# Optimization experiments

Measured on AMD Instinct MI355X. Metric: run time of the kernel, lower is better.

## Reference

```python
import jax, jax.numpy as jnp
import numpy as np

B, P, C, O = 16, 19248, 81, 32
POS_THRESH, NEG_THRESH, NEGPOS_RATIO = 0.5, 0.4, 3
BBOX_ALPHA, CONF_ALPHA = 1.5, 1.0
VAR0, VAR1 = 0.1, 0.2  # SSD encoding variances


def setup_inputs() -> dict:
    key = jax.random.key(0)
    ks = jax.random.split(key, 7)
    loc_data = jax.random.normal(ks[0], (B, P, 4), dtype=jnp.float32)
    conf_data = jax.random.normal(ks[1], (B, P, C), dtype=jnp.float32)
    # priors in center form (cx, cy, w, h), all positive
    cxcy = jax.random.uniform(ks[2], (P, 2), minval=0.05, maxval=0.95)
    wh = jax.random.uniform(ks[3], (P, 2), minval=0.05, maxval=0.30)
    priors = jnp.concatenate([cxcy, wh], axis=-1).astype(jnp.float32)
    # gt boxes in point form (x1, y1, x2, y2), valid and inside [0,1]
    gcxcy = jax.random.uniform(ks[4], (B, O, 2), minval=0.1, maxval=0.9)
    gwh = jax.random.uniform(ks[5], (B, O, 2), minval=0.05, maxval=0.4)
    gt_boxes = jnp.clip(jnp.concatenate([gcxcy - gwh / 2, gcxcy + gwh / 2], axis=-1), 0.0, 1.0).astype(jnp.float32)
    gt_labels = jax.random.randint(ks[6], (B, O), 0, C - 1, dtype=jnp.int32)  # 0..79, bg is class 0 after +1
    return {"loc_data": loc_data, "conf_data": conf_data, "priors": priors,
            "gt_boxes": gt_boxes, "gt_labels": gt_labels}


def _point_form(boxes):
    # center form (cx,cy,w,h) -> point form (x1,y1,x2,y2)
    return jnp.concatenate([boxes[:, :2] - boxes[:, 2:] / 2,
                            boxes[:, :2] + boxes[:, 2:] / 2], axis=-1)


def _jaccard(a, b):
    # a: [O,4] point form, b: [P,4] point form -> IoU [O,P]
    lt = jnp.maximum(a[:, None, :2], b[None, :, :2])
    rb = jnp.minimum(a[:, None, 2:], b[None, :, 2:])
    inter = jnp.prod(jnp.clip(rb - lt, 0.0, None), axis=-1)
    area_a = jnp.prod(a[:, 2:] - a[:, :2], axis=-1)[:, None]
    area_b = jnp.prod(b[:, 2:] - b[:, :2], axis=-1)[None, :]
    return inter / (area_a + area_b - inter)


def _encode(matched, priors):
    # matched: [P,4] point form gt; priors: [P,4] center form
    g_cxcy = ((matched[:, :2] + matched[:, 2:]) / 2 - priors[:, :2]) / (VAR0 * priors[:, 2:])
    g_wh = jnp.log((matched[:, 2:] - matched[:, :2]) / priors[:, 2:]) / VAR1
    return jnp.concatenate([g_cxcy, g_wh], axis=-1)


def _match_one(truths, labels, priors):
    # truths: [O,4] point form, labels: [O] int, priors: [P,4] center form
    overlaps = _jaccard(truths, _point_form(priors))          # [O,P]
    best_truth_overlap = overlaps.max(axis=0)                  # [P]
    best_truth_idx = overlaps.argmax(axis=0)                   # [P]
    best_prior_idx = overlaps.argmax(axis=1)                   # [O]
    # ensure every gt is matched to its best prior
    best_truth_overlap = best_truth_overlap.at[best_prior_idx].set(2.0)
    best_truth_idx = best_truth_idx.at[best_prior_idx].set(jnp.arange(truths.shape[0]))
    matched = truths[best_truth_idx]                           # [P,4]
    conf = labels[best_truth_idx] + 1                          # [P]
    conf = jnp.where(best_truth_overlap < POS_THRESH, -1, conf)  # neutral
    conf = jnp.where(best_truth_overlap < NEG_THRESH, 0, conf)   # background
    loc = _encode(matched, priors)                             # [P,4]
    return loc, conf


def _multibox_loss(loc_data, conf_data, priors, gt_boxes, gt_labels):
    loc_t, conf_t = jax.vmap(_match_one, in_axes=(0, 0, None))(gt_boxes, gt_labels, priors)
    pos = conf_t > 0                                           # [B,P]
    # --- localization: smooth L1 on positives ---
    d = jnp.abs(loc_data - loc_t)
    sl1 = jnp.where(d < 1.0, 0.5 * d * d, d - 0.5)
    loss_B = jnp.sum(sl1 * pos[..., None].astype(sl1.dtype)) * BBOX_ALPHA
    # --- OHEM confidence loss ---
    logZ = jax.nn.logsumexp(conf_data, axis=-1)                # [B,P]
    loss_c = logZ - conf_data[..., 0]                          # log_sum_exp - background logit
    loss_c = jnp.where(pos | (conf_t < 0), 0.0, loss_c)
    order = jnp.argsort(-loss_c, axis=1)                       # descending
    idx_rank = jnp.argsort(order, axis=1)                      # rank of each prior
    num_pos = jnp.sum(pos, axis=1, keepdims=True)              # [B,1]
    num_neg = jnp.clip(NEGPOS_RATIO * num_pos, None, P - 1)
    neg = (idx_rank < num_neg) & (~pos) & (conf_t >= 0)
    ce = logZ - jnp.take_along_axis(conf_data, jnp.maximum(conf_t, 0)[..., None], axis=-1)[..., 0]
    loss_C = jnp.sum(ce * (pos | neg).astype(ce.dtype)) * CONF_ALPHA
    total_num_pos = jnp.sum(pos).astype(loc_data.dtype)
    return jnp.stack([loss_B, loss_C]) / total_num_pos


def reference(loc_data, conf_data, priors, gt_boxes, gt_labels):
    return _multibox_loss(loc_data, conf_data, priors, gt_boxes, gt_labels)
```

## Files before the change

### kernel.cpp

```cpp
#include <hip/hip_runtime.h>
#include <math.h>

#define B_ 16
#define P_ 19248
#define C_ 81
#define O_ 32
#define POS_TH 0.5f
#define NEG_TH 0.4f
#define RPB 128
#define TPB 512
#define PQ  4812
#define BP_BLK (B_ * O_ * 4)
#define BT_BPB 76
#define OT 1024
#define NJ 19

__device__ __forceinline__ float sl1(float x) {
    float d = fabsf(x);
    return (d < 1.0f) ? 0.5f * d * d : d - 0.5f;
}

__device__ __forceinline__ float iou_gt_prior(float4 t, float4 pr) {
    float px1 = pr.x - pr.z * 0.5f;
    float py1 = pr.y - pr.w * 0.5f;
    float px2 = pr.x + pr.z * 0.5f;
    float py2 = pr.y + pr.w * 0.5f;
    float ltx = fmaxf(t.x, px1), lty = fmaxf(t.y, py1);
    float rbx = fminf(t.z, px2), rby = fminf(t.w, py2);
    float iw = fmaxf(rbx - ltx, 0.0f), ih = fmaxf(rby - lty, 0.0f);
    float inter = iw * ih;
    float area_t = (t.z - t.x) * (t.w - t.y);
    float area_p = (px2 - px1) * (py2 - py1);
    return inter / (area_t + area_p - inter);
}

template <int PER>
__device__ __forceinline__ void pick_top(const int* __restrict__ h, int kk, int tid,
                                         int* s_bin, int* s_kk, int* wsum) {
    const int lane = tid & 63, wid = tid >> 6;
    const int base = tid * PER;
    int v[PER]; int s = 0;
    #pragma unroll
    for (int j = 0; j < PER; ++j) { v[j] = h[base + j]; s += v[j]; }
    int x = s;
    #pragma unroll
    for (int d = 1; d < 64; d <<= 1) {
        int y = __shfl_down(x, d);
        if (lane + d < 64) x += y;
    }
    if (lane == 0) wsum[wid] = x;
    __syncthreads();
    int above = 0;
    #pragma unroll
    for (int w = 0; w < 16; ++w) if (w > wid) above += wsum[w];
    int T = (x - s) + above;
    if (T < kk && kk <= T + s) {
        int kl = kk - T, cum = 0;
        #pragma unroll
        for (int j = PER - 1; j >= 0; --j) {
            if (cum + v[j] >= kl) { *s_bin = base + j; *s_kk = kl - cum; break; }
            cum += v[j];
        }
    }
    __syncthreads();
}

template <int PER>
__device__ __forceinline__ void pick_bot(const int* __restrict__ h, int kk, int tid,
                                         int* s_bin, int* s_kk, int* wsum) {
    const int lane = tid & 63, wid = tid >> 6;
    const int base = tid * PER;
    int v[PER]; int s = 0;
    #pragma unroll
    for (int j = 0; j < PER; ++j) { v[j] = h[base + j]; s += v[j]; }
    int x = s;
    #pragma unroll
    for (int d = 1; d < 64; d <<= 1) {
        int y = __shfl_up(x, d);
        if (lane >= d) x += y;
    }
    if (lane == 63) wsum[wid] = x;
    __syncthreads();
    int below = 0;
    #pragma unroll
    for (int w = 0; w < 16; ++w) if (w < wid) below += wsum[w];
    int T = (x - s) + below;
    if (T < kk && kk <= T + s) {
        int kl = kk - T, cum = 0;
        #pragma unroll
        for (int j = 0; j < PER; ++j) {
            if (cum + v[j] >= kl) { *s_bin = base + j; *s_kk = kl - cum; break; }
            cum += v[j];
        }
    }
    __syncthreads();
}

__global__ void k_match(const float* __restrict__ priors,
                        const float* __restrict__ gt_boxes,
                        const int* __restrict__ gt_labels,
                        unsigned long long* __restrict__ best_key,
                        float* __restrict__ bt_ov,
                        int* __restrict__ bt_ix,
                        int* __restrict__ bt_lab) {
    const int bid = blockIdx.x;
    if (bid < BP_BLK) {
        int pair = bid >> 2, qtr = bid & 3;
        int b = pair >> 5, o = pair & 31;
        float4 t = ((const float4*)gt_boxes)[b * O_ + o];
        float bestv = -1.0f; int besti = 0;
        int pstart = qtr * PQ;
        for (int p = pstart + threadIdx.x; p < pstart + PQ; p += 256) {
            float4 pr = ((const float4*)priors)[p];
            float v = iou_gt_prior(t, pr);
            if (v > bestv) { bestv = v; besti = p; }
        }
        __shared__ float sv[256];
        __shared__ int   si[256];
        sv[threadIdx.x] = bestv; si[threadIdx.x] = besti;
        __syncthreads();
        for (int s = 128; s > 0; s >>= 1) {
            if (threadIdx.x < s) {
                float ov = sv[threadIdx.x + s]; int oi = si[threadIdx.x + s];
                if (ov > sv[threadIdx.x] ||
                    (ov == sv[threadIdx.x] && oi < si[threadIdx.x])) {
                    sv[threadIdx.x] = ov; si[threadIdx.x] = oi;
                }
            }
            __syncthreads();
        }
        if (threadIdx.x == 0) {
            unsigned long long key =
                ((unsigned long long)__float_as_uint(sv[0]) << 32) |
                (unsigned long long)(0xFFFFFFFFu - (unsigned int)si[0]);
            atomicMax(&best_key[pair], key);
        }
    } else {
        int idx = bid - BP_BLK;
        int b = idx / BT_BPB;
        int p = (idx % BT_BPB) * 256 + threadIdx.x;
        __shared__ float4 gt[O_];
        __shared__ int    gl[O_];
        if (threadIdx.x < O_) {
            gt[threadIdx.x] = ((const float4*)gt_boxes)[b * O_ + threadIdx.x];
            gl[threadIdx.x] = gt_labels[b * O_ + threadIdx.x];
        }
        __syncthreads();
        if (p >= P_) return;
        float4 pr = ((const float4*)priors)[p];
        float bestv = -1.0f; int besti = 0;
        for (int o = 0; o < O_; ++o) {
            float v = iou_gt_prior(gt[o], pr);
            if (v > bestv) { bestv = v; besti = o; }
        }
        size_t bp = (size_t)b * P_ + p;
        bt_ov[bp] = bestv;
        bt_ix[bp] = besti;
        bt_lab[bp] = gl[besti];
    }
}

__global__ __launch_bounds__(TPB, 6) void
k_main(const float* __restrict__ loc_data,
       const float* __restrict__ conf_data,
       const float* __restrict__ priors,
       const float* __restrict__ gt_boxes,
       const int* __restrict__ gt_labels,
       const unsigned long long* __restrict__ best_key,
       const float* __restrict__ bt_ov,
       const int* __restrict__ bt_ix,
       const int* __restrict__ bt_lab,
       float* __restrict__ lossc,
       float* __restrict__ ce_neg,
       int* __restrict__ num_pos,
       float* __restrict__ accum) {
    __shared__ float srow[RPB * C_];
    __shared__ int s_fp[2][O_];
    __shared__ int s_fl[2][O_];
    __shared__ float s_lB, s_ceP;
    __shared__ int s_np0, s_np1;
    const int row0 = blockIdx.x * RPB;
    const int b0 = row0 / P_;
    const int tid = threadIdx.x;
    const int w = tid >> 6;
    if (tid == 0) { s_lB = 0.0f; s_ceP = 0.0f; s_np0 = 0; s_np1 = 0; }

    {
        const float4* src = (const float4*)(conf_data + (size_t)row0 * C_);
        float4* dst4 = (float4*)srow;
        #pragma unroll
        for (int k = 0; k < 5; ++k) {
            __builtin_amdgcn_global_load_lds(
                (const __attribute__((address_space(1))) void*)(src + k * 512 + tid),
                (__attribute__((address_space(3))) void*)(dst4 + k * 512 + (w << 6)),
                16, 0, 0);
        }
        if (tid < 32) {
            __builtin_amdgcn_global_load_lds(
                (const __attribute__((address_space(1))) void*)(src + 2560 + tid),
                (__attribute__((address_space(3))) void*)(dst4 + 2560),
                16, 0, 0);
        }
    }
    if (tid < 2 * O_) {
        int half = tid >> 5, o = tid & 31;
        int bb = b0 + half;
        int fp = -1, fl = 0;
        if (bb < B_) {
            unsigned long long key = best_key[bb * O_ + o];
            fp = (int)(0xFFFFFFFFu - (unsigned int)(key & 0xFFFFFFFFu));
            fl = gt_labels[bb * O_ + o];
        }
        s_fp[half][o] = fp;
        s_fl[half][o] = fl;
    }
    __syncthreads();

    const int r = tid >> 2;
    const int q = tid & 3;
    const int bp = row0 + r;
    const int b = bp / P_;
    const int p = bp - b * P_;
    const float* row = srow + r * C_;
    const int j0 = 20 * q;

    float ma = row[j0], mb = row[j0 + 1], mc = row[j0 + 2], md = row[j0 + 3];
    #pragma unroll
    for (int i = 4; i < 20; i += 4) {
        ma = fmaxf(ma, row[j0 + i]);     mb = fmaxf(mb, row[j0 + i + 1]);
        mc = fmaxf(mc, row[j0 + i + 2]); md = fmaxf(md, row[j0 + i + 3]);
    }
    float m = fmaxf(fmaxf(ma, mb), fmaxf(mc, md));
    if (q == 3) m = fmaxf(m, row[80]);
    m = fmaxf(m, __shfl_xor(m, 1));
    m = fmaxf(m, __shfl_xor(m, 2));

    float sa = 0.f, sb = 0.f, sc = 0.f, sd = 0.f;
    #pragma unroll
    for (int i = 0; i < 20; i += 4) {
        sa += __expf(row[j0 + i] - m);     sb += __expf(row[j0 + i + 1] - m);
        sc += __expf(row[j0 + i + 2] - m); sd += __expf(row[j0 + i + 3] - m);
    }
    float s = (sa + sb) + (sc + sd);
    if (q == 3) s += __expf(row[80] - m);
    s += __shfl_xor(s, 1);
    s += __shfl_xor(s, 2);
    float logZ = m + __logf(s);

    if (q == 0) {
        const int whichb = b - b0;
        int foo = -1;
        #pragma unroll
        for (int oo = O_ - 1; oo >= 0; --oo) {
            if (foo < 0 && s_fp[whichb][oo] == p) foo = oo;
        }
        int conf_t, ti = 0;
        bool pos;
        if (foo >= 0) {
            conf_t = s_fl[whichb][foo] + 1;
            pos = true;
            ti = foo;
        } else {
            float ov = bt_ov[bp];
            conf_t = bt_lab[bp] + 1;
            if (ov < POS_TH) conf_t = -1;
            if (ov < NEG_TH) conf_t = 0;
            pos = conf_t > 0;
            if (pos) ti = bt_ix[bp];
        }

        float lc = (pos || conf_t < 0) ? 0.0f : (logZ - row[0]);
        int cls = pos ? conf_t : 0;
        float ce = logZ - row[cls];

        lossc[bp] = lc;
        ce_neg[bp] = (conf_t == 0) ? ce : 0.0f;

        if (pos) {
            float4 t = ((const float4*)gt_boxes)[b * O_ + ti];
            float4 pr = ((const float4*)priors)[p];
            float mcx = (t.x + t.z) * 0.5f;
            float mcy = (t.y + t.w) * 0.5f;
            float gx = (mcx - pr.x) / (0.1f * pr.z);
            float gy = (mcy - pr.y) / (0.1f * pr.w);
            float gw = logf((t.z - t.x) / pr.z) / 0.2f;
            float gh = logf((t.w - t.y) / pr.w) / 0.2f;
            float4 ld = ((const float4*)loc_data)[bp];
            float sc2 = sl1(ld.x - gx) + sl1(ld.y - gy) + sl1(ld.z - gw) + sl1(ld.w - gh);
            atomicAdd(&s_lB, sc2);
            atomicAdd(&s_ceP, ce);
            if (b == b0) atomicAdd(&s_np0, 1); else atomicAdd(&s_np1, 1);
        }
    }
    __syncthreads();
    if (tid == 0) {
        if (s_lB != 0.0f) atomicAdd(&accum[0], s_lB);
        if (s_ceP != 0.0f) atomicAdd(&accum[1], s_ceP);
        if (s_np0) atomicAdd(&num_pos[b0], s_np0);
        if (s_np1) atomicAdd(&num_pos[b0 + 1], s_np1);
    }
}

__global__ __launch_bounds__(OT) void
k_ohem(const float* __restrict__ lossc, const float* __restrict__ ce_neg,
       const int* __restrict__ num_pos, const float* __restrict__ accum,
       float* __restrict__ ce_sum, int* __restrict__ done,
       float* __restrict__ out) {
    const int b = blockIdx.x;
    const int tid = threadIdx.x;
    const float* lc = lossc + (size_t)b * P_;
    const float* cn = ce_neg + (size_t)b * P_;
    __shared__ int h[2048];
    __shared__ int wsum[16];
    __shared__ int s_bin, s_kk;
    __shared__ float red[OT];

    int k = 3 * num_pos[b];
    if (k > P_ - 1) k = P_ - 1;

    float result = 0.0f;
    if (k > 0) {
        unsigned int fb[NJ]; float cv[NJ];
        #pragma unroll
        for (int j = 0; j < NJ; ++j) {
            int i = tid + j * OT;
            bool valid = (i < P_);
            fb[j] = valid ? __float_as_uint(lc[i]) : 0u;
            cv[j] = valid ? cn[i] : 0.0f;
        }
        h[tid] = 0; h[tid + 1024] = 0;
        __syncthreads();
        #pragma unroll
        for (int j = 0; j < NJ; ++j) atomicAdd(&h[fb[j] >> 21], 1);
        __syncthreads();
        pick_top<2>(h, k, tid, &s_bin, &s_kk, wsum);
        const unsigned int T = (unsigned int)s_bin;
        int kk = s_kk;

        h[tid] = 0; h[tid + 1024] = 0;
        __syncthreads();
        float sum = 0.0f;
        #pragma unroll
        for (int j = 0; j < NJ; ++j) {
            unsigned int bin = fb[j] >> 21;
            if (bin > T) sum += cv[j];
            else if (bin == T) atomicAdd(&h[(fb[j] >> 10) & 2047], 1);
        }
        __syncthreads();
        pick_top<2>(h, kk, tid, &s_bin, &s_kk, wsum);
        const unsigned int pre21 = (T << 11) | (unsigned int)s_bin;
        kk = s_kk;

        h[tid] = 0; h[tid + 1024] = 0;
        __syncthreads();
        #pragma unroll
        for (int j = 0; j < NJ; ++j)
            if ((fb[j] >> 10) == pre21) atomicAdd(&h[fb[j] & 1023], 1);
        __syncthreads();
        pick_top<2>(h, kk, tid, &s_bin, &s_kk, wsum);
        const unsigned int V = (pre21 << 10) | (unsigned int)s_bin;
        const int ee = h[s_bin];
        kk = s_kk;

        if (kk == ee) {
            #pragma unroll
            for (int j = 0; j < NJ; ++j)
                if ((fb[j] >> 21) == T && fb[j] >= V) sum += cv[j];
        } else {
            h[tid] = 0; h[tid + 1024] = 0;
            __syncthreads();
            #pragma unroll
            for (int j = 0; j < NJ; ++j)
                if (fb[j] == V) atomicAdd(&h[(tid + j * OT) >> 6], 1);
            __syncthreads();
            pick_bot<2>(h, kk, tid, &s_bin, &s_kk, wsum);
            const int d6 = s_bin;
            kk = s_kk;
            h[tid] = 0; h[tid + 1024] = 0;
            __syncthreads();
            #pragma unroll
            for (int j = 0; j < NJ; ++j) {
                int i = tid + j * OT;
                if (fb[j] == V && (i >> 6) == d6) atomicAdd(&h[i & 63], 1);
            }
            __syncthreads();
            pick_bot<2>(h, kk, tid, &s_bin, &s_kk, wsum);
            const int Istar = (d6 << 6) | s_bin;
            #pragma unroll
            for (int j = 0; j < NJ; ++j) {
                int i = tid + j * OT;
                if ((fb[j] >> 21) == T && (fb[j] > V || (fb[j] == V && i <= Istar)))
                    sum += cv[j];
            }
        }

        red[tid] = sum;
        __syncthreads();
        for (int s = OT / 2; s > 0; s >>= 1) {
            if (tid < s) red[tid] += red[tid + s];
            __syncthreads();
        }
        result = red[0];
    }

    if (tid == 0) {
        ce_sum[b] = result;
        __threadfence();
        int old = atomicAdd(done, 1);
        if (old == B_ - 1) {
            __threadfence();
            int tp = 0; float ns = 0.0f;
            for (int bb = 0; bb < B_; ++bb) { tp += num_pos[bb]; ns += ce_sum[bb]; }
            float inv = 1.0f / (float)tp;
            out[0] = accum[0] * 1.5f * inv;
            out[1] = (accum[1] + ns) * inv;
        }
    }
}

extern "C" void kernel_launch(void* const* d_in, const int* in_sizes, int n_in,
                              void* d_out, int out_size, void* d_ws, size_t ws_size,
                              hipStream_t stream) {
    const float* loc    = (const float*)d_in[0];
    const float* conf   = (const float*)d_in[1];
    const float* priors = (const float*)d_in[2];
    const float* gtb    = (const float*)d_in[3];
    const int*   gtl    = (const int*)d_in[4];
    float* out = (float*)d_out;

    const size_t BP = (size_t)B_ * P_;
    float* W = (float*)d_ws;
    float* bt_ov   = W;
    float* lossc   = W + BP;
    float* ce_neg  = W + 2 * BP;
    int*   bt_ix   = (int*)(W + 3 * BP);
    int*   bt_lab  = (int*)(W + 4 * BP);
    unsigned long long* best_key = (unsigned long long*)(W + 5 * BP);
    int*   num_pos = (int*)(best_key + B_ * O_);
    float* ce_sum  = (float*)(num_pos + B_);
    float* accum   = ce_sum + B_;
    int*   done    = (int*)(accum + 2);

    size_t zbytes = B_ * O_ * sizeof(unsigned long long) +
                    B_ * sizeof(int) + B_ * sizeof(float) +
                    2 * sizeof(float) + sizeof(int);
    hipMemsetAsync(best_key, 0, zbytes, stream);
    hipLaunchKernelGGL(k_match, dim3(BP_BLK + B_ * BT_BPB), dim3(256), 0, stream,
                       priors, gtb, gtl, best_key, bt_ov, bt_ix, bt_lab);
    hipLaunchKernelGGL(k_main, dim3((int)(BP / RPB)), dim3(TPB), 0, stream,
                       loc, conf, priors, gtb, gtl, best_key,
                       bt_ov, bt_ix, bt_lab, lossc, ce_neg, num_pos, accum);
    hipLaunchKernelGGL(k_ohem, dim3(B_), dim3(OT), 0, stream,
                       lossc, ce_neg, num_pos, accum, ce_sum, done, out);
}
```

Baseline: 119.0 us.

## Fuse per-prior best-truth matching into main loss kernel

```diff
diff --git a/kernel.cpp b/kernel.cpp
--- a/kernel.cpp
+++ b/kernel.cpp
@@ -11,9 +11,11 @@
 #define TPB 512
 #define PQ  4812
 #define BP_BLK (B_ * O_ * 4)
-#define BT_BPB 76
 #define OT 1024
 #define NJ 19
+
+#define AS1 const __attribute__((address_space(1))) void*
+#define AS3 __attribute__((address_space(3))) void*
 
 __device__ __forceinline__ float sl1(float x) {
     float d = fabsf(x);
@@ -98,65 +100,37 @@
 
 __global__ void k_match(const float* __restrict__ priors,
                         const float* __restrict__ gt_boxes,
-                        const int* __restrict__ gt_labels,
-                        unsigned long long* __restrict__ best_key,
-                        float* __restrict__ bt_ov,
-                        int* __restrict__ bt_ix,
-                        int* __restrict__ bt_lab) {
+                        unsigned long long* __restrict__ best_key) {
     const int bid = blockIdx.x;
-    if (bid < BP_BLK) {
-        int pair = bid >> 2, qtr = bid & 3;
-        int b = pair >> 5, o = pair & 31;
-        float4 t = ((const float4*)gt_boxes)[b * O_ + o];
-        float bestv = -1.0f; int besti = 0;
-        int pstart = qtr * PQ;
-        for (int p = pstart + threadIdx.x; p < pstart + PQ; p += 256) {
-            float4 pr = ((const float4*)priors)[p];
-            float v = iou_gt_prior(t, pr);
-            if (v > bestv) { bestv = v; besti = p; }
-        }
-        __shared__ float sv[256];
-        __shared__ int   si[256];
-        sv[threadIdx.x] = bestv; si[threadIdx.x] = besti;
-        __syncthreads();
-        for (int s = 128; s > 0; s >>= 1) {
-            if (threadIdx.x < s) {
-                float ov = sv[threadIdx.x + s]; int oi = si[threadIdx.x + s];
-                if (ov > sv[threadIdx.x] ||
-                    (ov == sv[threadIdx.x] && oi < si[threadIdx.x])) {
-                    sv[threadIdx.x] = ov; si[threadIdx.x] = oi;
-                }
+    int pair = bid >> 2, qtr = bid & 3;
+    int b = pair >> 5, o = pair & 31;
+    float4 t = ((const float4*)gt_boxes)[b * O_ + o];
+    float bestv = -1.0f; int besti = 0;
+    int pstart = qtr * PQ;
+    for (int p = pstart + threadIdx.x; p < pstart + PQ; p += 256) {
+        float4 pr = ((const float4*)priors)[p];
+        float v = iou_gt_prior(t, pr);
+        if (v > bestv) { bestv = v; besti = p; }
+    }
+    __shared__ float sv[256];
+    __shared__ int   si[256];
+    sv[threadIdx.x] = bestv; si[threadIdx.x] = besti;
+    __syncthreads();
+    for (int s = 128; s > 0; s >>= 1) {
+        if (threadIdx.x < s) {
+            float ov = sv[threadIdx.x + s]; int oi = si[threadIdx.x + s];
+            if (ov > sv[threadIdx.x] ||
+                (ov == sv[threadIdx.x] && oi < si[threadIdx.x])) {
+                sv[threadIdx.x] = ov; si[threadIdx.x] = oi;
             }
-            __syncthreads();
-        }
-        if (threadIdx.x == 0) {
-            unsigned long long key =
-                ((unsigned long long)__float_as_uint(sv[0]) << 32) |
-                (unsigned long long)(0xFFFFFFFFu - (unsigned int)si[0]);
-            atomicMax(&best_key[pair], key);
-        }
-    } else {
-        int idx = bid - BP_BLK;
-        int b = idx / BT_BPB;
-        int p = (idx % BT_BPB) * 256 + threadIdx.x;
-        __shared__ float4 gt[O_];
-        __shared__ int    gl[O_];
-        if (threadIdx.x < O_) {
-            gt[threadIdx.x] = ((const float4*)gt_boxes)[b * O_ + threadIdx.x];
-            gl[threadIdx.x] = gt_labels[b * O_ + threadIdx.x];
-        }
-        __syncthreads();
-        if (p >= P_) return;
-        float4 pr = ((const float4*)priors)[p];
-        float bestv = -1.0f; int besti = 0;
-        for (int o = 0; o < O_; ++o) {
-            float v = iou_gt_prior(gt[o], pr);
-            if (v > bestv) { bestv = v; besti = o; }
-        }
-        size_t bp = (size_t)b * P_ + p;
-        bt_ov[bp] = bestv;
-        bt_ix[bp] = besti;
-        bt_lab[bp] = gl[besti];
+        }
+        __syncthreads();
+    }
+    if (threadIdx.x == 0) {
+        unsigned long long key =
+            ((unsigned long long)__float_as_uint(sv[0]) << 32) |
+            (unsigned long long)(0xFFFFFFFFu - (unsigned int)si[0]);
+        atomicMax(&best_key[pair], key);
     }
 }
 
@@ -167,14 +141,13 @@
        const float* __restrict__ gt_boxes,
        const int* __restrict__ gt_labels,
        const unsigned long long* __restrict__ best_key,
-       const float* __restrict__ bt_ov,
-       const int* __restrict__ bt_ix,
-       const int* __restrict__ bt_lab,
        float* __restrict__ lossc,
        float* __restrict__ ce_neg,
        int* __restrict__ num_pos,
        float* __restrict__ accum) {
     __shared__ float srow[RPB * C_];
+    __shared__ float4 s_gt[2][O_];
+    __shared__ int s_gl[2][O_];
     __shared__ int s_fp[2][O_];
     __shared__ int s_fl[2][O_];
     __shared__ float s_lB, s_ceP;
@@ -190,29 +163,32 @@
         float4* dst4 = (float4*)srow;
         #pragma unroll
         for (int k = 0; k < 5; ++k) {
-            __builtin_amdgcn_global_load_lds(
-                (const __attribute__((address_space(1))) void*)(src + k * 512 + tid),
-                (__attribute__((address_space(3))) void*)(dst4 + k * 512 + (w << 6)),
-                16, 0, 0);
+            __builtin_amdgcn_global_load_lds((AS1)(src + k * 512 + tid),
+                                             (AS3)(dst4 + k * 512 + (w << 6)),
+                                             16, 0, 0);
         }
         if (tid < 32) {
-            __builtin_amdgcn_global_load_lds(
-                (const __attribute__((address_space(1))) void*)(src + 2560 + tid),
-                (__attribute__((address_space(3))) void*)(dst4 + 2560),
-                16, 0, 0);
+            __builtin_amdgcn_global_load_lds((AS1)(src + 2560 + tid),
+                                             (AS3)(dst4 + 2560), 16, 0, 0);
         }
     }
     if (tid < 2 * O_) {
         int half = tid >> 5, o = tid & 31;
         int bb = b0 + half;
         int fp = -1, fl = 0;
+        float4 g = make_float4(0.f, 0.f, 0.f, 0.f);
+        int gl = 0;
         if (bb < B_) {
             unsigned long long key = best_key[bb * O_ + o];
             fp = (int)(0xFFFFFFFFu - (unsigned int)(key & 0xFFFFFFFFu));
             fl = gt_labels[bb * O_ + o];
+            g  = ((const float4*)gt_boxes)[bb * O_ + o];
+            gl = fl;
         }
         s_fp[half][o] = fp;
         s_fl[half][o] = fl;
+        s_gt[half][o] = g;
+        s_gl[half][o] = gl;
     }
     __syncthreads();
 
@@ -221,8 +197,24 @@
     const int bp = row0 + r;
     const int b = bp / P_;
     const int p = bp - b * P_;
+    const int whichb = b - b0;
     const float* row = srow + r * C_;
     const int j0 = 20 * q;
+
+    const float4 pr4 = ((const float4*)priors)[p];
+    float bestv = -1.0f; int besti = 0;
+    #pragma unroll
+    for (int oo = 0; oo < 8; ++oo) {
+        int g = 8 * q + oo;
+        float v = iou_gt_prior(s_gt[whichb][g], pr4);
+        if (v > bestv) { bestv = v; besti = g; }
+    }
+    #pragma unroll
+    for (int d = 1; d < 4; d <<= 1) {
+        float ov = __shfl_xor(bestv, d);
+        int oi = __shfl_xor(besti, d);
+        if (ov > bestv || (ov == bestv && oi < besti)) { bestv = ov; besti = oi; }
+    }
 
     float ma = row[j0], mb = row[j0 + 1], mc = row[j0 + 2], md = row[j0 + 3];
     #pragma unroll
@@ -248,25 +240,23 @@
     float logZ = m + __logf(s);
 
     if (q == 0) {
-        const int whichb = b - b0;
         int foo = -1;
         #pragma unroll
         for (int oo = O_ - 1; oo >= 0; --oo) {
             if (foo < 0 && s_fp[whichb][oo] == p) foo = oo;
         }
-        int conf_t, ti = 0;
+        int conf_t, ti;
         bool pos;
         if (foo >= 0) {
             conf_t = s_fl[whichb][foo] + 1;
             pos = true;
             ti = foo;
         } else {
-            float ov = bt_ov[bp];
-            conf_t = bt_lab[bp] + 1;
-            if (ov < POS_TH) conf_t = -1;
-            if (ov < NEG_TH) conf_t = 0;
+            conf_t = s_gl[whichb][besti] + 1;
+            if (bestv < POS_TH) conf_t = -1;
+            if (bestv < NEG_TH) conf_t = 0;
             pos = conf_t > 0;
-            if (pos) ti = bt_ix[bp];
+            ti = besti;
         }
 
         float lc = (pos || conf_t < 0) ? 0.0f : (logZ - row[0]);
@@ -277,14 +267,13 @@
         ce_neg[bp] = (conf_t == 0) ? ce : 0.0f;
 
         if (pos) {
-            float4 t = ((const float4*)gt_boxes)[b * O_ + ti];
-            float4 pr = ((const float4*)priors)[p];
+            float4 t = s_gt[whichb][ti];
             float mcx = (t.x + t.z) * 0.5f;
             float mcy = (t.y + t.w) * 0.5f;
-            float gx = (mcx - pr.x) / (0.1f * pr.z);
-            float gy = (mcy - pr.y) / (0.1f * pr.w);
-            float gw = logf((t.z - t.x) / pr.z) / 0.2f;
-            float gh = logf((t.w - t.y) / pr.w) / 0.2f;
+            float gx = (mcx - pr4.x) / (0.1f * pr4.z);
+            float gy = (mcy - pr4.y) / (0.1f * pr4.w);
+            float gw = logf((t.z - t.x) / pr4.z) / 0.2f;
+            float gh = logf((t.w - t.y) / pr4.w) / 0.2f;
             float4 ld = ((const float4*)loc_data)[bp];
             float sc2 = sl1(ld.x - gx) + sl1(ld.y - gy) + sl1(ld.z - gw) + sl1(ld.w - gh);
             atomicAdd(&s_lB, sc2);
@@ -430,12 +419,9 @@
 
     const size_t BP = (size_t)B_ * P_;
     float* W = (float*)d_ws;
-    float* bt_ov   = W;
-    float* lossc   = W + BP;
-    float* ce_neg  = W + 2 * BP;
-    int*   bt_ix   = (int*)(W + 3 * BP);
-    int*   bt_lab  = (int*)(W + 4 * BP);
-    unsigned long long* best_key = (unsigned long long*)(W + 5 * BP);
+    float* lossc   = W;
+    float* ce_neg  = W + BP;
+    unsigned long long* best_key = (unsigned long long*)(W + 2 * BP);
     int*   num_pos = (int*)(best_key + B_ * O_);
     float* ce_sum  = (float*)(num_pos + B_);
     float* accum   = ce_sum + B_;
@@ -445,11 +431,11 @@
                     B_ * sizeof(int) + B_ * sizeof(float) +
                     2 * sizeof(float) + sizeof(int);
     hipMemsetAsync(best_key, 0, zbytes, stream);
-    hipLaunchKernelGGL(k_match, dim3(BP_BLK + B_ * BT_BPB), dim3(256), 0, stream,
-                       priors, gtb, gtl, best_key, bt_ov, bt_ix, bt_lab);
+    hipLaunchKernelGGL(k_match, dim3(BP_BLK), dim3(256), 0, stream,
+                       priors, gtb, best_key);
     hipLaunchKernelGGL(k_main, dim3((int)(BP / RPB)), dim3(TPB), 0, stream,
                        loc, conf, priors, gtb, gtl, best_key,
-                       bt_ov, bt_ix, bt_lab, lossc, ce_neg, num_pos, accum);
+                       lossc, ce_neg, num_pos, accum);
     hipLaunchKernelGGL(k_ohem, dim3(B_), dim3(OT), 0, stream,
                        lossc, ce_neg, num_pos, accum, ce_sum, done, out);
 }
```

After: 114.8 us. 1.04x faster.
